# Kernel optimization log

Hardware: AMD Instinct MI355X
Metric: run time of the kernel (lower is better)

## Reference

```python
import jax, jax.numpy as jnp
import numpy as np

D_MODEL = 1024
N_HEADS = 16
HEAD_DIM = D_MODEL // N_HEADS  # 64
D_LATENT = 4 * (D_MODEL // 4)  # 1024
LN_EPS = 1e-5
NORM_EPS = 1e-12


def setup_inputs() -> dict:
    key = jax.random.key(0)
    ks = jax.random.split(key, 20)
    B, S = 2, 2048
    s = lambda fan_in: 1.0 / np.sqrt(fan_in)
    inp = {
        "query": jax.random.normal(ks[0], (B, S, D_MODEL), jnp.float32),
        "key_in": jax.random.normal(ks[1], (B, S, D_MODEL), jnp.float32),
        "value": jax.random.normal(ks[2], (B, S, D_MODEL), jnp.float32),
        # z_proj
        "Wz": jax.random.uniform(ks[3], (D_MODEL, D_LATENT), jnp.float32, -s(D_MODEL), s(D_MODEL)),
        "bz": jax.random.uniform(ks[4], (D_LATENT,), jnp.float32, -s(D_MODEL), s(D_MODEL)),
        # z_norm (LayerNorm)
        "ln_g": jnp.ones((D_LATENT,), jnp.float32),
        "ln_b": jnp.zeros((D_LATENT,), jnp.float32),
        # q/r/h projections: d_latent -> n_heads*head_dim
        "Wq": jax.random.uniform(ks[5], (D_LATENT, N_HEADS * HEAD_DIM), jnp.float32, -s(D_LATENT), s(D_LATENT)),
        "bq": jax.random.uniform(ks[6], (N_HEADS * HEAD_DIM,), jnp.float32, -s(D_LATENT), s(D_LATENT)),
        "Wr": jax.random.uniform(ks[7], (D_LATENT, N_HEADS * HEAD_DIM), jnp.float32, -s(D_LATENT), s(D_LATENT)),
        "br": jax.random.uniform(ks[8], (N_HEADS * HEAD_DIM,), jnp.float32, -s(D_LATENT), s(D_LATENT)),
        "Wh": jax.random.uniform(ks[9], (D_LATENT, N_HEADS * HEAD_DIM), jnp.float32, -s(D_LATENT), s(D_LATENT)),
        "bh": jax.random.uniform(ks[10], (N_HEADS * HEAD_DIM,), jnp.float32, -s(D_LATENT), s(D_LATENT)),
        # phi_proj: head_dim -> head_dim (shared across heads, applied to Q and R)
        "Wphi": jax.random.uniform(ks[11], (HEAD_DIM, HEAD_DIM), jnp.float32, -s(HEAD_DIM), s(HEAD_DIM)),
        "bphi": jax.random.uniform(ks[12], (HEAD_DIM,), jnp.float32, -s(HEAD_DIM), s(HEAD_DIM)),
        # out_proj
        "Wo": jax.random.uniform(ks[13], (D_MODEL, D_MODEL), jnp.float32, -s(D_MODEL), s(D_MODEL)),
        "bo": jax.random.uniform(ks[14], (D_MODEL,), jnp.float32, -s(D_MODEL), s(D_MODEL)),
    }
    return inp


def reference(query, key_in, value, Wz, bz, ln_g, ln_b, Wq, bq, Wr, br, Wh, bh, Wphi, bphi, Wo, bo):
    # NOTE: the original module ignores key_in and value entirely.
    B, S, _ = query.shape
    # latent projection + LayerNorm
    Z = query @ Wz + bz
    mu = jnp.mean(Z, axis=-1, keepdims=True)
    var = jnp.mean(jnp.square(Z - mu), axis=-1, keepdims=True)
    Z = (Z - mu) * jax.lax.rsqrt(var + LN_EPS) * ln_g + ln_b
    # Q, R, H projections -> [B, S, H, D]
    Q = (Z @ Wq + bq).reshape(B, S, N_HEADS, HEAD_DIM)
    R = (Z @ Wr + br).reshape(B, S, N_HEADS, HEAD_DIM)
    Hv = (Z @ Wh + bh).reshape(B, S, N_HEADS, HEAD_DIM)
    # phasor activation Psi(v) = v * exp(i * (v Wphi + bphi))
    phiQ = Q @ Wphi + bphi
    phiR = R @ Wphi + bphi
    # Re(Q' conj(R')) = (Q cos phiQ)(R cos phiR) + (Q sin phiQ)(R sin phiR)
    # stack real/imag components along head_dim so a single einsum gives the real part
    Qc = jnp.concatenate([Q * jnp.cos(phiQ), Q * jnp.sin(phiQ)], axis=-1)  # [B,S,H,2D]
    Rc = jnp.concatenate([R * jnp.cos(phiR), R * jnp.sin(phiR)], axis=-1)  # [B,S,H,2D]
    scores = jnp.einsum('bqhd,bkhd->bhqk', Qc, Rc)  # real part of complex QK^H
    # L2 row-normalization (torch F.normalize p=2 dim=-1, eps=1e-12)
    norm = jnp.sqrt(jnp.sum(jnp.square(scores), axis=-1, keepdims=True))
    attn = scores / jnp.maximum(norm, NORM_EPS)
    out = jnp.einsum('bhqk,bkhd->bqhd', attn, Hv).reshape(B, S, D_MODEL)
    return out @ Wo + bo
```

## Files before the change

### kernel.cpp

```cpp
#include <hip/hip_runtime.h>

#define DEV __device__ __forceinline__

typedef __bf16 bf16x8 __attribute__((ext_vector_type(8)));
typedef float f32x4 __attribute__((ext_vector_type(4)));

DEV float b2f(__bf16 v) { return (float)v; }
DEV __bf16 f2b(float v) { return (__bf16)v; }

DEV void gload16(const __bf16* g, __bf16* l) {
  __builtin_amdgcn_global_load_lds((const __attribute__((address_space(1))) unsigned*)g,
                                   (__attribute__((address_space(3))) unsigned*)l, 16, 0, 0);
}

__global__ void detect_k(const unsigned short* __restrict__ q, int* __restrict__ mode) {
  const int lane = threadIdx.x & 63;
  int cntNaN = 0, cntSmall = 0;
  for (int i = lane; i < 16384; i += 64) {
    const unsigned ef = (q[i] >> 7) & 0xFF;
    if (ef == 0xFF) cntNaN++;
    if (ef < 0x70) cntSmall++;
  }
#pragma unroll
  for (int o = 32; o > 0; o >>= 1) {
    cntNaN += __shfl_down(cntNaN, o);
    cntSmall += __shfl_down(cntSmall, o);
  }
  if (lane == 0) *mode = (cntNaN >= 4) ? 1 : ((cntSmall > 2000) ? 2 : 0);
}

__global__ __launch_bounds__(256) void qcvt_k(const void* __restrict__ src,
                                              __bf16* __restrict__ dst,
                                              int n8, const int* __restrict__ mode) {
  const int i = blockIdx.x * 256 + threadIdx.x;
  if (i >= n8) return;
  const int m = *mode;
  union { __bf16 h[8]; int4 u; } pk;
  if (m == 1) {
    const float4* p = (const float4*)src + (size_t)i * 2;
    const float4 a = p[0], b = p[1];
    pk.h[0] = f2b(a.x); pk.h[1] = f2b(a.y); pk.h[2] = f2b(a.z); pk.h[3] = f2b(a.w);
    pk.h[4] = f2b(b.x); pk.h[5] = f2b(b.y); pk.h[6] = f2b(b.z); pk.h[7] = f2b(b.w);
  } else if (m == 2) {
    const _Float16* p = (const _Float16*)src + (size_t)i * 8;
#pragma unroll
    for (int t = 0; t < 8; t++) pk.h[t] = f2b((float)p[t]);
  } else {
    pk.u = ((const int4*)src)[i];
  }
  ((int4*)dst)[i] = pk.u;
}

struct CvtJobs {
  const void* src[9];
  __bf16* dst[9];
};
__global__ __launch_bounds__(256) void cvt_all_k(CvtJobs J, const int* __restrict__ mode) {
  const int bb = blockIdx.x;
  int job, off;
  if (bb < 4) { job = bb; off = 0; }
  else if (bb == 4) { job = 4; off = 0; }
  else if (bb < 9) { job = 5; off = (bb - 5) * 1024; }
  else { job = 6 + (bb - 9); off = 0; }
  const int n = (job == 4) ? 64 : (job == 5) ? 4096 : 1024;
  const int m = *mode;
  const void* s = J.src[job];
  __bf16* d = J.dst[job];
  const int rem = n - off;
  const int cnt = rem > 1024 ? 1024 : rem;
  for (int i = threadIdx.x; i < cnt; i += 256) {
    const int idx = off + i;
    const float v = (m == 1) ? ((const float*)s)[idx]
                  : (m == 2) ? (float)((const _Float16*)s)[idx]
                             : b2f(((const __bf16*)s)[idx]);
    d[idx] = f2b(v);
  }
}

struct TJobs {
  const void* src[5];
  __bf16* dst[5];
};
__global__ __launch_bounds__(256) void tcvt_all_k(TJobs J, const int* __restrict__ mode) {
  __shared__ __bf16 tile[64][68];
  const void* in = J.src[blockIdx.z];
  __bf16* out = J.dst[blockIdx.z];
  const int c0 = blockIdx.x * 64, r0 = blockIdx.y * 64;
  const int tid = threadIdx.x;
  const int m = *mode;
  for (int i = tid; i < 64 * 16; i += 256) {
    int r = i >> 4, cc = (i & 15) * 4;
    const size_t base = (size_t)(r0 + r) * 1024 + c0 + cc;
    if (m == 1) {
      float4 v = *(const float4*)((const float*)in + base);
      tile[r][cc + 0] = f2b(v.x);
      tile[r][cc + 1] = f2b(v.y);
      tile[r][cc + 2] = f2b(v.z);
      tile[r][cc + 3] = f2b(v.w);
    } else if (m == 2) {
      const _Float16* p = (const _Float16*)in + base;
      tile[r][cc + 0] = f2b((float)p[0]);
      tile[r][cc + 1] = f2b((float)p[1]);
      tile[r][cc + 2] = f2b((float)p[2]);
      tile[r][cc + 3] = f2b((float)p[3]);
    } else {
      *(uint2*)&tile[r][cc] = *(const uint2*)((const __bf16*)in + base);
    }
  }
  __syncthreads();
  for (int i = tid; i < 64 * 16; i += 256) {
    int c = i >> 4, rr = (i & 15) * 4;
    union { __bf16 h[4]; uint2 u; } pk;
    pk.h[0] = tile[rr + 0][c];
    pk.h[1] = tile[rr + 1][c];
    pk.h[2] = tile[rr + 2][c];
    pk.h[3] = tile[rr + 3][c];
    *(uint2*)&out[(size_t)(c0 + c) * 1024 + r0 + rr] = pk.u;
  }
}

template <bool OUT_F32>
__global__ __launch_bounds__(256) void gemm2p_k(const __bf16* __restrict__ A,
                                                const __bf16* __restrict__ BT,
                                                const __bf16* __restrict__ bias,
                                                void* __restrict__ Cout,
                                                int M, int N, int K) {
  __shared__ __bf16 As[2][64 * 64];
  __shared__ __bf16 Bs[2][64 * 64];
  const int tid = threadIdx.x, lane = tid & 63, wv = tid >> 6;
  const int quad = lane >> 4, l16 = lane & 15;
  const int nblk = gridDim.x, chunk = nblk >> 3;
  const int hb = blockIdx.x;
  const int lb = (hb & 7) * chunk + (hb >> 3);
  const int mcnt = M >> 6;
  const int ni = lb / mcnt, mi = lb - ni * mcnt;
  const int m0 = mi * 64, n0 = ni * 64;
  const int wm = (wv >> 1) * 32, wn = (wv & 1) * 32;

  int s_src[2];
#pragma unroll
  for (int u = 0; u < 2; u++) {
    const int ci = tid + u * 256;
    const int r = ci >> 3, cc = ci & 7;
    s_src[u] = r * K + ((cc ^ (r & 7)) * 8);
  }

#define GSTAGE(BUF, K0)                                                   \
  {                                                                       \
    const __bf16* a_ = A + (size_t)m0 * K + (K0);                         \
    const __bf16* b_ = BT + (size_t)n0 * K + (K0);                        \
    gload16(a_ + s_src[0], &As[BUF][tid * 8]);                            \
    gload16(a_ + s_src[1], &As[BUF][(tid + 256) * 8]);                    \
    gload16(b_ + s_src[0], &Bs[BUF][tid * 8]);                            \
    gload16(b_ + s_src[1], &Bs[BUF][(tid + 256) * 8]);                    \
  }

  f32x4 acc[2][2] = {};
  const int nk = K >> 6;
  const int key = l16 & 7;

  GSTAGE(0, 0);
  __syncthreads();

  for (int t = 0; t < nk; ++t) {
    const int cur = t & 1;
    if (t + 1 < nk) GSTAGE(cur ^ 1, (t + 1) * 64);
#pragma unroll
    for (int s = 0; s < 2; s++) {
      const int co = ((4 * s + quad) ^ key) * 8;
      bf16x8 af[2], bfr[2];
#pragma unroll
      for (int i = 0; i < 2; i++) af[i] = *(const bf16x8*)&As[cur][(wm + i * 16 + l16) * 64 + co];
#pragma unroll
      for (int j = 0; j < 2; j++) bfr[j] = *(const bf16x8*)&Bs[cur][(wn + j * 16 + l16) * 64 + co];
#pragma unroll
      for (int i = 0; i < 2; i++)
#pragma unroll
        for (int j = 0; j < 2; j++)
          acc[i][j] = __builtin_amdgcn_mfma_f32_16x16x32_bf16(af[i], bfr[j], acc[i][j], 0, 0, 0);
    }
    __syncthreads();
  }
#undef GSTAGE

#pragma unroll
  for (int j = 0; j < 2; j++) {
    const int col = n0 + wn + j * 16 + l16;
    const float bv = b2f(bias[col]);
#pragma unroll
    for (int i = 0; i < 2; i++) {
#pragma unroll
      for (int r = 0; r < 4; r++) {
        const int row = m0 + wm + i * 16 + quad * 4 + r;
        const float v = acc[i][j][r] + bv;
        if (OUT_F32)
          ((float*)Cout)[(size_t)row * N + col] = v;
        else
          ((__bf16*)Cout)[(size_t)row * N + col] = f2b(v);
      }
    }
  }
}

__global__ __launch_bounds__(256) void qrh2p_k(const __bf16* __restrict__ A,
                                               const __bf16* __restrict__ BT3,
                                               const __bf16* __restrict__ bias3,
                                               __bf16* __restrict__ Qf,
                                               __bf16* __restrict__ Rf,
                                               __bf16* __restrict__ Hv,
                                               int M) {
  __shared__ __bf16 As[2][64 * 64];
  __shared__ __bf16 Bs[2][128 * 64];
  const int tid = threadIdx.x, lane = tid & 63, wv = tid >> 6;
  const int quad = lane >> 4, l16 = lane & 15;
  const int nblk = gridDim.x, chunk = nblk >> 3;
  const int hb = blockIdx.x;
  const int lb = (hb & 7) * chunk + (hb >> 3);
  const int mcnt = M >> 6;
  const int ni = lb / mcnt, mi = lb - ni * mcnt;
  const int m0 = mi * 64, n0g = ni * 128;
  const int which = n0g >> 10, n0 = n0g & 1023;
  __bf16* out = (which == 0) ? Qf : (which == 1) ? Rf : Hv;
  const int wm = (wv >> 1) * 32, wn = (wv & 1) * 64;
  const int K = 1024;

  int s_src[4];
#pragma unroll
  for (int u = 0; u < 4; u++) {
    const int ci = tid + u * 256;
    const int r = ci >> 3, cc = ci & 7;
    s_src[u] = r * K + ((cc ^ (r & 7)) * 8);
  }

#define GSTAGE(BUF, K0)                                                   \
  {                                                                       \
    const __bf16* a_ = A + (size_t)m0 * K + (K0);                         \
    const __bf16* b_ = BT3 + (size_t)n0g * K + (K0);                      \
    gload16(a_ + s_src[0], &As[BUF][tid * 8]);                            \
    gload16(a_ + s_src[1], &As[BUF][(tid + 256) * 8]);                    \
    _Pragma("unroll")                                                     \
    for (int u = 0; u < 4; u++)                                           \
      gload16(b_ + s_src[u], &Bs[BUF][(tid + u * 256) * 8]);              \
  }

  f32x4 acc[2][4] = {};
  const int key = l16 & 7;

  GSTAGE(0, 0);
  __syncthreads();

  for (int t = 0; t < 16; ++t) {
    const int cur = t & 1;
    if (t + 1 < 16) GSTAGE(cur ^ 1, (t + 1) * 64);
#pragma unroll
    for (int s = 0; s < 2; s++) {
      const int co = ((4 * s + quad) ^ key) * 8;
      bf16x8 af[2], bfr[4];
#pragma unroll
      for (int i = 0; i < 2; i++) af[i] = *(const bf16x8*)&As[cur][(wm + i * 16 + l16) * 64 + co];
#pragma unroll
      for (int j = 0; j < 4; j++) bfr[j] = *(const bf16x8*)&Bs[cur][(wn + j * 16 + l16) * 64 + co];
#pragma unroll
      for (int i = 0; i < 2; i++)
#pragma unroll
        for (int j = 0; j < 4; j++)
          acc[i][j] = __builtin_amdgcn_mfma_f32_16x16x32_bf16(af[i], bfr[j], acc[i][j], 0, 0, 0);
    }
    __syncthreads();
  }
#undef GSTAGE

#pragma unroll
  for (int j = 0; j < 4; j++) {
    const int colg = n0g + wn + j * 16 + l16;
    const int col = n0 + wn + j * 16 + l16;
    const float bv = b2f(bias3[colg]);
#pragma unroll
    for (int i = 0; i < 2; i++) {
#pragma unroll
      for (int r = 0; r < 4; r++) {
        const int row = m0 + wm + i * 16 + quad * 4 + r;
        out[(size_t)row * 1024 + col] = f2b(acc[i][j][r] + bv);
      }
    }
  }
}

__global__ __launch_bounds__(256) void ln_k(const float* __restrict__ Zraw,
                                            const __bf16* __restrict__ g,
                                            const __bf16* __restrict__ bb,
                                            __bf16* __restrict__ Z) {
  __shared__ float red[8];
  const int row = blockIdx.x, tid = threadIdx.x, lane = tid & 63, wv = tid >> 6;
  const float* x = Zraw + (size_t)row * 1024;
  float4 v = *(const float4*)&x[tid * 4];
  float s = v.x + v.y + v.z + v.w;
  float ss = v.x * v.x + v.y * v.y + v.z * v.z + v.w * v.w;
#pragma unroll
  for (int o = 32; o > 0; o >>= 1) {
    s += __shfl_down(s, o);
    ss += __shfl_down(ss, o);
  }
  if (lane == 0) { red[wv] = s; red[4 + wv] = ss; }
  __syncthreads();
  const float S = red[0] + red[1] + red[2] + red[3];
  const float SS = red[4] + red[5] + red[6] + red[7];
  const float mu = S * (1.f / 1024.f);
  const float var = SS * (1.f / 1024.f) - mu * mu;
  const float rstd = rsqrtf(var + 1e-5f);
  const int c = tid * 4;
  float xs[4] = {v.x, v.y, v.z, v.w};
  union { __bf16 h[4]; uint2 u; } pk;
#pragma unroll
  for (int i = 0; i < 4; i++)
    pk.h[i] = f2b((xs[i] - mu) * rstd * b2f(g[c + i]) + b2f(bb[c + i]));
  *(uint2*)&Z[(size_t)row * 1024 + c] = pk.u;
}

__global__ __launch_bounds__(256) void phasor_mfma_k(const __bf16* __restrict__ Qf,
                                                     const __bf16* __restrict__ Rf,
                                                     const __bf16* __restrict__ Wphi,
                                                     const __bf16* __restrict__ bphi,
                                                     __bf16* __restrict__ Qc,
                                                     __bf16* __restrict__ Rc) {
  __shared__ __bf16 Qs[128][76];
  __shared__ __bf16 WT[64][76];
  const __bf16* in = blockIdx.y ? Rf : Qf;
  __bf16* out = blockIdx.y ? Rc : Qc;
  const int tid = threadIdx.x, lane = tid & 63, wv = tid >> 6;
  const int quad = lane >> 4, l16 = lane & 15;
  const size_t m0 = (size_t)blockIdx.x * 128;
  for (int i = tid; i < 1024; i += 256) {
    int r = i >> 3, c = (i & 7) * 8;
    *(int4*)&Qs[r][c] = *(const int4*)&in[(m0 + r) * 64 + c];
  }
  for (int i = tid; i < 4096; i += 256) WT[i & 63][i >> 6] = Wphi[i];
  __syncthreads();
  f32x4 acc[2][4] = {};
#pragma unroll
  for (int s = 0; s < 2; s++) {
    const int ka = s * 32 + quad * 8;
    bf16x8 bfr[4];
#pragma unroll
    for (int j = 0; j < 4; j++) bfr[j] = *(const bf16x8*)&WT[j * 16 + l16][ka];
#pragma unroll
    for (int i = 0; i < 2; i++) {
      const bf16x8 af = *(const bf16x8*)&Qs[wv * 32 + i * 16 + l16][ka];
#pragma unroll
      for (int j = 0; j < 4; j++)
        acc[i][j] = __builtin_amdgcn_mfma_f32_16x16x32_bf16(af, bfr[j], acc[i][j], 0, 0, 0);
    }
  }
#pragma unroll
  for (int i = 0; i < 2; i++)
#pragma unroll
    for (int j = 0; j < 4; j++) {
      const int col = j * 16 + l16;
      const float bj = b2f(bphi[col]);
#pragma unroll
      for (int r = 0; r < 4; r++) {
        const int row = wv * 32 + i * 16 + quad * 4 + r;
        const float phi = acc[i][j][r] + bj;
        float sn, cs;
        __sincosf(phi, &sn, &cs);
        const float qv = b2f(Qs[row][col]);
        const size_t ob = (m0 + row) * 128;
        out[ob + col] = f2b(qv * cs);
        out[ob + 64 + col] = f2b(qv * sn);
      }
    }
}

__global__ __launch_bounds__(256) void hvt_k(const __bf16* __restrict__ Hv,
                                             __bf16* __restrict__ HvT, int S) {
  __shared__ __bf16 t[64][72];
  const int tt = blockIdx.x * 64, h = blockIdx.y, b = blockIdx.z;
  const int tid = threadIdx.x;
  for (int i = tid; i < 512; i += 256) {
    int tok = i >> 3, dc = (i & 7) * 8;
    *(int4*)&t[tok][dc] = *(const int4*)&Hv[((size_t)(b * S + tt + tok) * 16 + h) * 64 + dc];
  }
  __syncthreads();
  for (int i = tid; i < 1024; i += 256) {
    int d = i >> 4, tc = (i & 15) * 4;
    union { __bf16 h4[4]; uint2 u; } pk;
    pk.h4[0] = t[tc + 0][d];
    pk.h4[1] = t[tc + 1][d];
    pk.h4[2] = t[tc + 2][d];
    pk.h4[3] = t[tc + 3][d];
    *(uint2*)&HvT[(((size_t)(b * 16 + h) * 64 + d) * S) + tt + tc] = pk.u;
  }
}

__global__ __launch_bounds__(256) void attn_k(const __bf16* __restrict__ Qc,
                                              const __bf16* __restrict__ Rc,
                                              const __bf16* __restrict__ HvT,
                                              __bf16* __restrict__ Aout, int S) {
  __shared__ __bf16 Rs[2][64 * 128];
  __shared__ __bf16 Hs[2][64 * 64];
  const int tid = threadIdx.x, lane = tid & 63, wv = tid >> 6;
  const int quad = lane >> 4, l16 = lane & 15;
  const int nblk = gridDim.x;
  const int chunk = nblk >> 3;
  const int hb = blockIdx.x;
  const int lb = (hb & 7) * chunk + (hb >> 3);
  const int nx = nblk >> 5;
  const int x = lb % nx;
  const int rest = lb / nx;
  const int h = rest & 15, b = rest >> 4;
  const int q0 = x * 128;

  bf16x8 qf[2][4];
#pragma unroll
  for (int i = 0; i < 2; i++) {
    const __bf16* qp = Qc + ((size_t)(b * S + q0 + wv * 32 + i * 16 + l16) * 16 + h) * 128 + quad * 8;
#pragma unroll
    for (int s = 0; s < 4; s++) qf[i][s] = *(const bf16x8*)(qp + s * 32);
  }

  const size_t rcb = ((size_t)b * S * 16 + h) * 128;
  const size_t hvb = (size_t)(b * 16 + h) * 64 * S;

  int rs_src[4], hs_src[2];
#pragma unroll
  for (int u = 0; u < 4; u++) {
    const int r = 4 * (wv * 4 + u) + (lane >> 4);
    rs_src[u] = r * 2048 + (((lane & 15) ^ (r & 7)) * 8);
  }
#pragma unroll
  for (int u = 0; u < 2; u++) {
    const int row = 8 * (wv * 2 + u) + (lane >> 3);
    hs_src[u] = row * S + (((lane & 7) ^ (row & 7)) * 8);
  }

#define STAGE(BUF, TILE)                                                        \
  {                                                                             \
    const __bf16* rc_ = Rc + rcb + (size_t)(TILE) * 64 * 2048;                  \
    const __bf16* hv_ = HvT + hvb + (TILE) * 64;                                \
    _Pragma("unroll")                                                           \
    for (int u = 0; u < 4; u++)                                                 \
      gload16(rc_ + rs_src[u], &Rs[BUF][(wv * 4 + u) * 512]);                   \
    _Pragma("unroll")                                                           \
    for (int u = 0; u < 2; u++)                                                 \
      gload16(hv_ + hs_src[u], &Hs[BUF][(wv * 2 + u) * 512]);                   \
  }

  f32x4 oacc[2][4] = {};
  float rssq[2] = {};
  const int nt = S >> 6;

  STAGE(0, 0);
  __syncthreads();

  const int srcA = ((quad & 1) << 1) | (quad >> 1);
  const int adA = ((srcA << 4) | l16) << 2;
  const int adB = (((srcA ^ 1) << 4) | l16) << 2;
  const bool par = (quad & 1) != 0;
  const bool hi = (quad >> 1) != 0;
  const int key = l16 & 7;

  for (int it = 0; it < nt; ++it) {
    const int cur = it & 1;
    if (it + 1 < nt) STAGE(cur ^ 1, it + 1);

    f32x4 sacc[4][2] = {};
#pragma unroll
    for (int s = 0; s < 4; s++) {
      const int co = ((4 * s + quad) ^ key) * 8;
#pragma unroll
      for (int jt = 0; jt < 4; jt++) {
        const bf16x8 rf = *(const bf16x8*)&Rs[cur][(jt * 16 + l16) * 128 + co];
#pragma unroll
        for (int i = 0; i < 2; i++)
          sacc[jt][i] = __builtin_amdgcn_mfma_f32_16x16x32_bf16(rf, qf[i][s], sacc[jt][i], 0, 0, 0);
      }
    }

    unsigned pk[4][2][2];
#pragma unroll
    for (int jt = 0; jt < 4; jt++)
#pragma unroll
      for (int i = 0; i < 2; i++) {
        rssq[i] += sacc[jt][i][0] * sacc[jt][i][0] + sacc[jt][i][1] * sacc[jt][i][1] +
                   sacc[jt][i][2] * sacc[jt][i][2] + sacc[jt][i][3] * sacc[jt][i][3];
        union { __bf16 h2[2]; unsigned u; } p0, p1;
        p0.h2[0] = f2b(sacc[jt][i][0]); p0.h2[1] = f2b(sacc[jt][i][1]);
        p1.h2[0] = f2b(sacc[jt][i][2]); p1.h2[1] = f2b(sacc[jt][i][3]);
        pk[jt][i][0] = p0.u; pk[jt][i][1] = p1.u;
      }

#pragma unroll
    for (int s2 = 0; s2 < 2; s2++) {
      bf16x8 hf[4];
      const int co2 = ((4 * s2 + quad) ^ key) * 8;
#pragma unroll
      for (int jd = 0; jd < 4; jd++)
        hf[jd] = *(const bf16x8*)&Hs[cur][(jd * 16 + l16) * 64 + co2];
      const int jA = 2 * s2, jB = 2 * s2 + 1;
#pragma unroll
      for (int i = 0; i < 2; i++) {
        const unsigned o0 = par ? pk[jB][i][0] : pk[jA][i][0];
        const unsigned o1 = par ? pk[jB][i][1] : pk[jA][i][1];
        const unsigned o2 = par ? pk[jA][i][0] : pk[jB][i][0];
        const unsigned o3 = par ? pk[jA][i][1] : pk[jB][i][1];
        const unsigned r0 = (unsigned)__builtin_amdgcn_ds_bpermute(adA, (int)o0);
        const unsigned r1 = (unsigned)__builtin_amdgcn_ds_bpermute(adA, (int)o1);
        const unsigned r2 = (unsigned)__builtin_amdgcn_ds_bpermute(adB, (int)o2);
        const unsigned r3 = (unsigned)__builtin_amdgcn_ds_bpermute(adB, (int)o3);
        union { unsigned u[4]; bf16x8 v; } bw;
        bw.u[0] = hi ? r2 : r0;
        bw.u[1] = hi ? r3 : r1;
        bw.u[2] = hi ? r0 : r2;
        bw.u[3] = hi ? r1 : r3;
#pragma unroll
        for (int jd = 0; jd < 4; jd++)
          oacc[i][jd] = __builtin_amdgcn_mfma_f32_16x16x32_bf16(hf[jd], bw.v, oacc[i][jd], 0, 0, 0);
      }
    }
    __syncthreads();
  }
#undef STAGE

#pragma unroll
  for (int i = 0; i < 2; i++) {
    float t = rssq[i];
    t += __shfl_xor(t, 16);
    t += __shfl_xor(t, 32);
    const float inv = 1.0f / fmaxf(sqrtf(t), 1e-12f);
    const size_t orow = (size_t)(b * S + q0 + wv * 32 + i * 16 + l16) * 1024 + h * 64;
#pragma unroll
    for (int jd = 0; jd < 4; jd++) {
      union { __bf16 h4[4]; uint2 u2; } o;
#pragma unroll
      for (int r = 0; r < 4; r++) o.h4[r] = f2b(oacc[i][jd][r] * inv);
      *(uint2*)&Aout[orow + jd * 16 + quad * 4] = o.u2;
    }
  }
}

extern "C" void kernel_launch(void* const* d_in, const int* in_sizes, int n_in,
                              void* d_out, int out_size, void* d_ws, size_t ws_size,
                              hipStream_t stream) {
  const void* query = d_in[0];
  const void* Wz = d_in[3];
  const void* bz = d_in[4];
  const void* ln_g = d_in[5];
  const void* ln_b = d_in[6];
  const void* Wq = d_in[7];
  const void* bq = d_in[8];
  const void* Wr = d_in[9];
  const void* br = d_in[10];
  const void* Wh = d_in[11];
  const void* bh = d_in[12];
  const void* Wphi = d_in[13];
  const void* bphi = d_in[14];
  const void* Wo = d_in[15];
  const void* bo = d_in[16];

  const int n_q = in_sizes[0];
  const int Srows = n_q >> 10;
  const int S = Srows >> 1;

  char* ws = (char*)d_ws;
  const size_t MB = 1024 * 1024;

  int* mode = (int*)(ws);
  __bf16* sv = (__bf16*)(ws + 4096);
  __bf16* bz_c   = sv + 0 * 4096;
  __bf16* lng_c  = sv + 1 * 4096;
  __bf16* lnb_c  = sv + 2 * 4096;
  __bf16* bo_c   = sv + 3 * 4096;
  __bf16* bphi_c = sv + 4 * 4096;
  __bf16* wphi_c = sv + 5 * 4096;
  __bf16* bqrh   = sv + 6 * 4096;
  __bf16* WzT    = (__bf16*)(ws + 1 * MB);
  __bf16* WoT    = (__bf16*)(ws + 3 * MB);
  __bf16* WqrhT  = (__bf16*)(ws + 5 * MB);
  float*  Zraw   = (float*) (ws + 11 * MB);
  __bf16* Z      = (__bf16*)(ws + 27 * MB);
  __bf16* Qf     = (__bf16*)(ws + 35 * MB);
  __bf16* Rf     = (__bf16*)(ws + 43 * MB);
  __bf16* Hv     = (__bf16*)(ws + 51 * MB);
  __bf16* Qbf    = (__bf16*)(ws + 59 * MB);
  __bf16* Rc     = (__bf16*)(ws + 59 * MB);
  __bf16* Qc     = (__bf16*)(ws + 11 * MB);
  __bf16* HvT    = (__bf16*)(ws + 27 * MB);
  __bf16* Aout   = (__bf16*)(ws + 35 * MB);

  dim3 blk(256);
  detect_k<<<1, 64, 0, stream>>>((const unsigned short*)query, mode);

  CvtJobs cj;
  cj.src[0] = bz;   cj.dst[0] = bz_c;
  cj.src[1] = ln_g; cj.dst[1] = lng_c;
  cj.src[2] = ln_b; cj.dst[2] = lnb_c;
  cj.src[3] = bo;   cj.dst[3] = bo_c;
  cj.src[4] = bphi; cj.dst[4] = bphi_c;
  cj.src[5] = Wphi; cj.dst[5] = wphi_c;
  cj.src[6] = bq;   cj.dst[6] = bqrh;
  cj.src[7] = br;   cj.dst[7] = bqrh + 1024;
  cj.src[8] = bh;   cj.dst[8] = bqrh + 2048;
  cvt_all_k<<<12, blk, 0, stream>>>(cj, mode);

  TJobs tj;
  tj.src[0] = Wz; tj.dst[0] = WzT;
  tj.src[1] = Wo; tj.dst[1] = WoT;
  tj.src[2] = Wq; tj.dst[2] = WqrhT;
  tj.src[3] = Wr; tj.dst[3] = WqrhT + 1024 * 1024;
  tj.src[4] = Wh; tj.dst[4] = WqrhT + 2 * 1024 * 1024;
  tcvt_all_k<<<dim3(16, 16, 5), blk, 0, stream>>>(tj, mode);

  qcvt_k<<<(Srows * 1024 / 8 + 255) / 256, blk, 0, stream>>>(query, Qbf, Srows * 128, mode);

  const int mcnt = Srows / 64;
  gemm2p_k<true><<<16 * mcnt, blk, 0, stream>>>(Qbf, WzT, bz_c, (void*)Zraw,
                                                Srows, 1024, 1024);
  ln_k<<<Srows, blk, 0, stream>>>(Zraw, lng_c, lnb_c, Z);
  qrh2p_k<<<24 * mcnt, blk, 0, stream>>>(Z, WqrhT, bqrh, Qf, Rf, Hv, Srows);
  phasor_mfma_k<<<dim3((Srows * 16) / 128, 2), blk, 0, stream>>>(Qf, Rf, wphi_c, bphi_c, Qc, Rc);
  hvt_k<<<dim3(S / 64, 16, 2), blk, 0, stream>>>(Hv, HvT, S);
  attn_k<<<dim3((S / 128) * 32), blk, 0, stream>>>(Qc, Rc, HvT, Aout, S);
  gemm2p_k<true><<<16 * mcnt, blk, 0, stream>>>(Aout, WoT, bo_c, d_out,
                                                Srows, 1024, 1024);
}
```

Baseline: 311.4 us.

## Software-pipeline attention loop with triple-buffered LDS and skewed QK/PV stages

Restructures the attention main loop so the PV matmul for tile i-1 is issued alongside the QK matmul for tile i. LDS buffers go from two to three, and the full __syncthreads is replaced by explicit vmcnt waits plus a raw s_barrier. The aim is to keep MFMA units busy while global-to-LDS loads are in flight and to remove one barrier stall per tile. The cost is more LDS use, which may reduce occupancy, two sets of packed score registers, and hand-tuned waitcnt counts that must match the number of outstanding loads.

```diff
diff --git a/kernel.cpp b/kernel.cpp
--- a/kernel.cpp
+++ b/kernel.cpp
@@ -396,8 +396,8 @@
                                               const __bf16* __restrict__ Rc,
                                               const __bf16* __restrict__ HvT,
                                               __bf16* __restrict__ Aout, int S) {
-  __shared__ __bf16 Rs[2][64 * 128];
-  __shared__ __bf16 Hs[2][64 * 64];
+  __shared__ __bf16 Rs[3][64 * 128];
+  __shared__ __bf16 Hs[3][64 * 64];
   const int tid = threadIdx.x, lane = tid & 63, wv = tid >> 6;
   const int quad = lane >> 4, l16 = lane & 15;
   const int nblk = gridDim.x;
@@ -450,7 +450,6 @@
   const int nt = S >> 6;
 
   STAGE(0, 0);
-  __syncthreads();
 
   const int srcA = ((quad & 1) << 1) | (quad >> 1);
   const int adA = ((srcA << 4) | l16) << 2;
@@ -459,67 +458,107 @@
   const bool hi = (quad >> 1) != 0;
   const int key = l16 & 7;
 
-  for (int it = 0; it < nt; ++it) {
-    const int cur = it & 1;
-    if (it + 1 < nt) STAGE(cur ^ 1, it + 1);
-
-    f32x4 sacc[4][2] = {};
-#pragma unroll
-    for (int s = 0; s < 4; s++) {
-      const int co = ((4 * s + quad) ^ key) * 8;
-#pragma unroll
-      for (int jt = 0; jt < 4; jt++) {
-        const bf16x8 rf = *(const bf16x8*)&Rs[cur][(jt * 16 + l16) * 128 + co];
-#pragma unroll
-        for (int i = 0; i < 2; i++)
-          sacc[jt][i] = __builtin_amdgcn_mfma_f32_16x16x32_bf16(rf, qf[i][s], sacc[jt][i], 0, 0, 0);
+  unsigned pkA[4][2][2], pkB[4][2][2];
+
+#define QKPACK(PKARR)                                                             \
+  {                                                                               \
+    f32x4 sacc[4][2] = {};                                                        \
+    _Pragma("unroll")                                                             \
+    for (int s = 0; s < 4; s++) {                                                 \
+      const int co = ((4 * s + quad) ^ key) * 8;                                  \
+      _Pragma("unroll")                                                           \
+      for (int jt = 0; jt < 4; jt++) {                                            \
+        const bf16x8 rf = *(const bf16x8*)&Rs[cur][(jt * 16 + l16) * 128 + co];   \
+        _Pragma("unroll")                                                         \
+        for (int i = 0; i < 2; i++)                                               \
+          sacc[jt][i] = __builtin_amdgcn_mfma_f32_16x16x32_bf16(rf, qf[i][s],     \
+                                                               sacc[jt][i], 0, 0, 0); \
+      }                                                                           \
+    }                                                                             \
+    _Pragma("unroll")                                                             \
+    for (int jt = 0; jt < 4; jt++)                                                \
+      _Pragma("unroll")                                                           \
+      for (int i = 0; i < 2; i++) {                                               \
+        rssq[i] += sacc[jt][i][0] * sacc[jt][i][0] + sacc[jt][i][1] * sacc[jt][i][1] + \
+                   sacc[jt][i][2] * sacc[jt][i][2] + sacc[jt][i][3] * sacc[jt][i][3];  \
+        union { __bf16 h2[2]; unsigned u; } p0_, p1_;                             \
+        p0_.h2[0] = f2b(sacc[jt][i][0]); p0_.h2[1] = f2b(sacc[jt][i][1]);         \
+        p1_.h2[0] = f2b(sacc[jt][i][2]); p1_.h2[1] = f2b(sacc[jt][i][3]);         \
+        PKARR[jt][i][0] = p0_.u; PKARR[jt][i][1] = p1_.u;                         \
+      }                                                                           \
+  }
+
+#define PVSTEP(PKARR, PBUF)                                                       \
+  _Pragma("unroll")                                                               \
+  for (int s2 = 0; s2 < 2; s2++) {                                                \
+    bf16x8 hf[4];                                                                 \
+    const int co2 = ((4 * s2 + quad) ^ key) * 8;                                  \
+    _Pragma("unroll")                                                             \
+    for (int jd = 0; jd < 4; jd++)                                                \
+      hf[jd] = *(const bf16x8*)&Hs[PBUF][(jd * 16 + l16) * 64 + co2];             \
+    const int jA = 2 * s2, jB = 2 * s2 + 1;                                       \
+    _Pragma("unroll")                                                             \
+    for (int i = 0; i < 2; i++) {                                                 \
+      const unsigned o0 = par ? PKARR[jB][i][0] : PKARR[jA][i][0];                \
+      const unsigned o1 = par ? PKARR[jB][i][1] : PKARR[jA][i][1];                \
+      const unsigned o2 = par ? PKARR[jA][i][0] : PKARR[jB][i][0];                \
+      const unsigned o3 = par ? PKARR[jA][i][1] : PKARR[jB][i][1];                \
+      const unsigned r0 = (unsigned)__builtin_amdgcn_ds_bpermute(adA, (int)o0);   \
+      const unsigned r1 = (unsigned)__builtin_amdgcn_ds_bpermute(adA, (int)o1);   \
+      const unsigned r2 = (unsigned)__builtin_amdgcn_ds_bpermute(adB, (int)o2);   \
+      const unsigned r3 = (unsigned)__builtin_amdgcn_ds_bpermute(adB, (int)o3);   \
+      union { unsigned u[4]; bf16x8 v; } bw;                                      \
+      bw.u[0] = hi ? r2 : r0;                                                     \
+      bw.u[1] = hi ? r3 : r1;                                                     \
+      bw.u[2] = hi ? r0 : r2;                                                     \
+      bw.u[3] = hi ? r1 : r3;                                                     \
+      _Pragma("unroll")                                                           \
+      for (int jd = 0; jd < 4; jd++)                                              \
+        oacc[i][jd] = __builtin_amdgcn_mfma_f32_16x16x32_bf16(hf[jd], bw.v,       \
+                                                             oacc[i][jd], 0, 0, 0); \
+    }                                                                             \
+  }
+
+  int cur = 0;
+  for (int it2 = 0; it2 < nt; it2 += 2) {
+    {
+      int nxt = cur + 1; if (nxt == 3) nxt = 0;
+      STAGE(nxt, it2 + 1);
+      if (it2 > 0) {
+        const int pb = (cur >= 1) ? cur - 1 : cur + 2;
+        PVSTEP(pkB, pb)
       }
-    }
-
-    unsigned pk[4][2][2];
-#pragma unroll
-    for (int jt = 0; jt < 4; jt++)
-#pragma unroll
-      for (int i = 0; i < 2; i++) {
-        rssq[i] += sacc[jt][i][0] * sacc[jt][i][0] + sacc[jt][i][1] * sacc[jt][i][1] +
-                   sacc[jt][i][2] * sacc[jt][i][2] + sacc[jt][i][3] * sacc[jt][i][3];
-        union { __bf16 h2[2]; unsigned u; } p0, p1;
-        p0.h2[0] = f2b(sacc[jt][i][0]); p0.h2[1] = f2b(sacc[jt][i][1]);
-        p1.h2[0] = f2b(sacc[jt][i][2]); p1.h2[1] = f2b(sacc[jt][i][3]);
-        pk[jt][i][0] = p0.u; pk[jt][i][1] = p1.u;
+      asm volatile("s_waitcnt vmcnt(6)" ::: "memory");
+      __builtin_amdgcn_s_barrier();
+      __builtin_amdgcn_sched_barrier(0);
+      QKPACK(pkA)
+      cur = nxt;
+    }
+    {
+      int nxt = cur + 1; if (nxt == 3) nxt = 0;
+      const bool last = (it2 + 2 >= nt);
+      if (!last) STAGE(nxt, it2 + 2);
+      {
+        const int pb = (cur >= 1) ? cur - 1 : cur + 2;
+        PVSTEP(pkA, pb)
       }
-
-#pragma unroll
-    for (int s2 = 0; s2 < 2; s2++) {
-      bf16x8 hf[4];
-      const int co2 = ((4 * s2 + quad) ^ key) * 8;
-#pragma unroll
-      for (int jd = 0; jd < 4; jd++)
-        hf[jd] = *(const bf16x8*)&Hs[cur][(jd * 16 + l16) * 64 + co2];
-      const int jA = 2 * s2, jB = 2 * s2 + 1;
-#pragma unroll
-      for (int i = 0; i < 2; i++) {
-        const unsigned o0 = par ? pk[jB][i][0] : pk[jA][i][0];
-        const unsigned o1 = par ? pk[jB][i][1] : pk[jA][i][1];
-        const unsigned o2 = par ? pk[jA][i][0] : pk[jB][i][0];
-        const unsigned o3 = par ? pk[jA][i][1] : pk[jB][i][1];
-        const unsigned r0 = (unsigned)__builtin_amdgcn_ds_bpermute(adA, (int)o0);
-        const unsigned r1 = (unsigned)__builtin_amdgcn_ds_bpermute(adA, (int)o1);
-        const unsigned r2 = (unsigned)__builtin_amdgcn_ds_bpermute(adB, (int)o2);
-        const unsigned r3 = (unsigned)__builtin_amdgcn_ds_bpermute(adB, (int)o3);
-        union { unsigned u[4]; bf16x8 v; } bw;
-        bw.u[0] = hi ? r2 : r0;
-        bw.u[1] = hi ? r3 : r1;
-        bw.u[2] = hi ? r0 : r2;
-        bw.u[3] = hi ? r1 : r3;
-#pragma unroll
-        for (int jd = 0; jd < 4; jd++)
-          oacc[i][jd] = __builtin_amdgcn_mfma_f32_16x16x32_bf16(hf[jd], bw.v, oacc[i][jd], 0, 0, 0);
-      }
-    }
-    __syncthreads();
+      if (!last)
+        asm volatile("s_waitcnt vmcnt(6)" ::: "memory");
+      else
+        asm volatile("s_waitcnt vmcnt(0)" ::: "memory");
+      __builtin_amdgcn_s_barrier();
+      __builtin_amdgcn_sched_barrier(0);
+      QKPACK(pkB)
+      cur = nxt;
+    }
+  }
+  {
+    const int pb = (cur >= 1) ? cur - 1 : cur + 2;
+    PVSTEP(pkB, pb)
   }
 #undef STAGE
+#undef QKPACK
+#undef PVSTEP
 
 #pragma unroll
   for (int i = 0; i < 2; i++) {
```

Measured after the change: 316.6 us. No clear change (+1.7%).
